# Kernel tuning notes

Hardware: AMD Instinct MI355X
Metric: run time of the kernel (lower is better)

Reference implementation:

```python
import jax, jax.numpy as jnp
import numpy as np

B, T, E = 8, 2048, 1024  # batch, seq_len, emb_size (= output_emb_size)


def setup_inputs() -> dict:
    key = jax.random.key(0)
    k1, k2, k3, k4, k5, k6, k7 = jax.random.split(key, 7)
    return {
        "q": jax.random.normal(k1, (B, T, E), jnp.float32),
        "k": jax.random.normal(k2, (B, T, E), jnp.float32),
        "v": jax.random.normal(k3, (B, T, E), jnp.float32),
        "mask": jax.random.randint(k4, (T, T), 0, 2, jnp.int32),
        # nn.Linear weights, stored [out, in] as in torch; applied as x @ W.T
        "Wq": jax.random.normal(k5, (E, E), jnp.float32) / np.sqrt(E),
        "Wk": jax.random.normal(k6, (E, E), jnp.float32) / np.sqrt(E),
        "Wv": jax.random.normal(k7, (E, E), jnp.float32) / np.sqrt(E),
    }


def reference(q, k, v, mask, Wq, Wk, Wv):
    # QKV projections (bias-free Linear): x @ W.T
    query = jnp.einsum("bte,oe->bto", q, Wq)
    key_p = jnp.einsum("bse,oe->bso", k, Wk)
    value = jnp.einsum("bse,oe->bso", v, Wv)
    d = key_p.shape[-1]
    scores = jnp.einsum("bto,bso->bts", query, key_p) / np.sqrt(d).astype(jnp.float32)
    # torch.any(mask): mask is nonzero somewhere -> apply masked_fill(mask==0, -inf)
    scores = jnp.where(mask[None, :, :] == 0, -jnp.inf, scores)
    weights = jax.nn.softmax(scores, axis=-1)
    return jnp.einsum("bts,bso->bto", weights, value)
```

## Files before the change

### kernel.cpp

```cpp
#include <hip/hip_runtime.h>
#include <hip/hip_bf16.h>

typedef __attribute__((ext_vector_type(8))) short short8;
typedef __attribute__((ext_vector_type(8))) unsigned short ushortx8;
typedef __attribute__((ext_vector_type(4))) unsigned short ushortx4;
typedef __attribute__((ext_vector_type(4))) float floatx4;

#define NB 8
#define NT 2048
#define NE 1024

__device__ __forceinline__ unsigned short f2bf(float f){
  unsigned int u = __builtin_bit_cast(unsigned int, f);
  u += 0x7FFFu + ((u >> 16) & 1u);
  return (unsigned short)(u >> 16);
}
__device__ __forceinline__ float bf2f(unsigned short h){
  unsigned int u = ((unsigned int)h) << 16;
  return __builtin_bit_cast(float, u);
}

__device__ __forceinline__ void async16(void* lds, const void* g){
  __builtin_amdgcn_global_load_lds(
      (const __attribute__((address_space(1))) unsigned int*)g,
      (__attribute__((address_space(3))) unsigned int*)lds, 16, 0, 0);
}

#define MFMA16(d, va, vb) \
  d = __builtin_amdgcn_mfma_f32_16x16x32_bf16(va, vb, d, 0, 0, 0)

__global__ __launch_bounds__(256) void cvt3(const float* __restrict__ a0,
                                            const float* __restrict__ a1,
                                            const float* __restrict__ a2,
                                            unsigned short* __restrict__ out,
                                            int n4_per){
  const float* src = blockIdx.y == 0 ? a0 : (blockIdx.y == 1 ? a1 : a2);
  unsigned short* dst = out + (size_t)blockIdx.y * (size_t)n4_per * 4;
  int i = blockIdx.x * 256 + threadIdx.x;
  if (i < n4_per){
    floatx4 f = ((const floatx4*)src)[i];
    ushortx4 o;
    o.x = f2bf(f.x); o.y = f2bf(f.y); o.z = f2bf(f.z); o.w = f2bf(f.w);
    *(ushortx4*)(dst + (size_t)i * 4) = o;
  }
}

__global__ __launch_bounds__(256) void pack_mask(const int* __restrict__ m,
                                                 unsigned long long* __restrict__ bits){
  int t = blockIdx.x * 256 + threadIdx.x;
  const int4* p = (const int4*)(m + (size_t)t * 64);
  unsigned long long w = 0;
  #pragma unroll
  for (int jj = 0; jj < 16; jj++){
    int4 v = p[jj];
    w |= (unsigned long long)(v.x != 0) << (jj * 4 + 0);
    w |= (unsigned long long)(v.y != 0) << (jj * 4 + 1);
    w |= (unsigned long long)(v.z != 0) << (jj * 4 + 2);
    w |= (unsigned long long)(v.w != 0) << (jj * 4 + 3);
  }
  bits[t] = w;
}

template<int EPI>
__global__ __launch_bounds__(512, 2) void gemm_nt(
    const unsigned short* __restrict__ A, long strideA,
    const unsigned short* __restrict__ B, long strideB,
    void* __restrict__ Out, long strideOutBytes,
    const unsigned long long* __restrict__ mbits,
    float* __restrict__ rowsums,
    int K, int gx, int gy)
{
  __shared__ __attribute__((aligned(16))) char Lds[131072];
  const int tid = threadIdx.x;
  const int lane = tid & 63, wave = tid >> 6;

  int L = blockIdx.x;
  int xcd = L & 7, tt = L >> 3;
  int x = tt % gx;
  int strip = xcd + ((tt / gx) << 3);
  int y = strip % gy, z = strip / gy;
  const int m0 = y << 8, n0 = x << 8;
  const int Nn = gx << 8;

  const unsigned short* Az = A + (size_t)z * strideA;
  const unsigned short* Bz = B + (size_t)z * strideB;

  const long rowb  = (long)K * 2;
  const long rs128 = rowb << 7;
  const int r0 = tid >> 2;
  const int c0 = (tid & 3) ^ ((r0 >> 1) & 3);
  const char* pA0 = (const char*)Az + (size_t)(m0 + r0) * rowb + (c0 << 4);
  const char* pA1 = pA0 + 64;
  const char* pB0 = (const char*)Bz + (size_t)(n0 + r0) * rowb + (c0 << 4);
  const char* pB1 = pB0 + 64;
  const int stg = tid << 4;

  auto stageU = [&](const char*& g, int ldsoff){
    async16(Lds + ldsoff + stg,        g);
    async16(Lds + ldsoff + stg + 8192, g + rs128);
    g += 128;
  };

  const int lm = lane & 15, qd = lane >> 4;
  const int wm = wave >> 2, wn = wave & 3;
  const int fsw  = (qd ^ ((lm >> 1) & 3)) << 4;
  const int aoff = ((wm << 7) + lm) * 64 + fsw;
  const int boff = 32768 + ((wn << 6) + lm) * 64 + fsw;

  floatx4 acc[8][4];
  floatx4 zero4 = {0.f, 0.f, 0.f, 0.f};
  #pragma unroll
  for (int a = 0; a < 8; a++)
    #pragma unroll
    for (int b = 0; b < 4; b++) acc[a][b] = zero4;

  const int NK = K >> 6;

  stageU(pB0, 32768);
  stageU(pA0, 0);
  stageU(pB1, 32768 + 16384);
  stageU(pA1, 16384);
  stageU(pB0, 65536 + 32768);
  stageU(pA0, 65536);
  stageU(pB1, 65536 + 32768 + 16384);
  asm volatile("s_waitcnt vmcnt(6)\n\ts_barrier" ::: "memory");

  short8 a[4], b[4];
  for (int t = 0; t < NK; ++t){
    const int rb = (t & 1) << 16;
    const int sb = rb ^ 65536;

    if (t + 1 < NK) stageU(pA1, sb + 16384);
    #pragma unroll
    for (int j = 0; j < 4; j++) a[j] = *(const short8*)(Lds + rb + aoff + j * 1024);
    #pragma unroll
    for (int n = 0; n < 4; n++) b[n] = *(const short8*)(Lds + rb + boff + n * 1024);
    asm volatile("s_waitcnt lgkmcnt(0)\n\ts_barrier" ::: "memory");
    __builtin_amdgcn_sched_barrier(0);
    __builtin_amdgcn_s_setprio(1);
    #pragma unroll
    for (int j = 0; j < 4; j++)
      #pragma unroll
      for (int n = 0; n < 4; n++) MFMA16(acc[j][n], a[j], b[n]);
    __builtin_amdgcn_s_setprio(0);

    if (t + 2 < NK) stageU(pB0, rb + 32768);
    #pragma unroll
    for (int j = 0; j < 4; j++) a[j] = *(const short8*)(Lds + rb + aoff + (4 + j) * 1024);
    if (t + 2 < NK)
      asm volatile("s_waitcnt vmcnt(10) lgkmcnt(0)\n\ts_barrier" ::: "memory");
    else if (t + 1 < NK)
      asm volatile("s_waitcnt vmcnt(8) lgkmcnt(0)\n\ts_barrier" ::: "memory");
    else
      asm volatile("s_waitcnt lgkmcnt(0)\n\ts_barrier" ::: "memory");
    __builtin_amdgcn_sched_barrier(0);
    __builtin_amdgcn_s_setprio(1);
    #pragma unroll
    for (int j = 0; j < 4; j++)
      #pragma unroll
      for (int n = 0; n < 4; n++) MFMA16(acc[4 + j][n], a[j], b[n]);
    __builtin_amdgcn_s_setprio(0);

    if (t + 2 < NK) stageU(pA0, rb);
    #pragma unroll
    for (int j = 0; j < 4; j++) a[j] = *(const short8*)(Lds + rb + 16384 + aoff + j * 1024);
    #pragma unroll
    for (int n = 0; n < 4; n++) b[n] = *(const short8*)(Lds + rb + 16384 + boff + n * 1024);
    asm volatile("s_waitcnt lgkmcnt(0)\n\ts_barrier" ::: "memory");
    __builtin_amdgcn_sched_barrier(0);
    __builtin_amdgcn_s_setprio(1);
    #pragma unroll
    for (int j = 0; j < 4; j++)
      #pragma unroll
      for (int n = 0; n < 4; n++) MFMA16(acc[j][n], a[j], b[n]);
    __builtin_amdgcn_s_setprio(0);

    #pragma unroll
    for (int j = 0; j < 4; j++) a[j] = *(const short8*)(Lds + rb + 16384 + aoff + (4 + j) * 1024);
    if (t + 2 < NK){
      stageU(pB1, rb + 32768 + 16384);
      asm volatile("s_waitcnt vmcnt(8) lgkmcnt(0)\n\ts_barrier" ::: "memory");
    } else {
      asm volatile("s_waitcnt vmcnt(0) lgkmcnt(0)\n\ts_barrier" ::: "memory");
    }
    __builtin_amdgcn_sched_barrier(0);
    __builtin_amdgcn_s_setprio(1);
    #pragma unroll
    for (int j = 0; j < 4; j++)
      #pragma unroll
      for (int n = 0; n < 4; n++) MFMA16(acc[4 + j][n], a[j], b[n]);
    __builtin_amdgcn_s_setprio(0);
  }

  char* OutZ = (char*)Out + (size_t)z * strideOutBytes;
  const int colbase = n0 + (wn << 6);
  if constexpr (EPI == 1){
    const int wcol = colbase >> 6;
    #pragma unroll
    for (int mi = 0; mi < 8; mi++){
      #pragma unroll
      for (int i = 0; i < 4; i++){
        int row = m0 + (wm << 7) + mi * 16 + qd * 4 + i;
        unsigned long long w = mbits[(size_t)row * (NT / 64) + wcol];
        unsigned short* po = (unsigned short*)OutZ + (size_t)row * Nn + colbase;
        float rsum = 0.f;
        #pragma unroll
        for (int ni = 0; ni < 4; ni++){
          float vv = acc[mi][ni][i];
          float e = ((w >> (ni * 16 + lm)) & 1ull) ? __expf(vv * 0.03125f) : 0.f;
          rsum += e;
          po[ni * 16 + lm] = f2bf(e);
        }
        rsum += __shfl_xor(rsum, 1, 64);
        rsum += __shfl_xor(rsum, 2, 64);
        rsum += __shfl_xor(rsum, 4, 64);
        rsum += __shfl_xor(rsum, 8, 64);
        if (lm == 0) atomicAdd(rowsums + ((size_t)z << 11) + row, rsum);
      }
    }
  } else if constexpr (EPI == 2){
    #pragma unroll
    for (int mi = 0; mi < 8; mi++){
      #pragma unroll
      for (int i = 0; i < 4; i++){
        int row = m0 + (wm << 7) + mi * 16 + qd * 4 + i;
        float inv = 1.0f / rowsums[((size_t)z << 11) + row];
        #pragma unroll
        for (int ni = 0; ni < 4; ni++){
          int col = colbase + ni * 16 + lm;
          ((float*)OutZ)[(size_t)row * Nn + col] = acc[mi][ni][i] * inv;
        }
      }
    }
  } else {
    #pragma unroll
    for (int mi = 0; mi < 8; mi++){
      #pragma unroll
      for (int i = 0; i < 4; i++){
        int row = m0 + (wm << 7) + mi * 16 + qd * 4 + i;
        #pragma unroll
        for (int ni = 0; ni < 4; ni++){
          int col = colbase + ni * 16 + lm;
          ((unsigned short*)OutZ)[(size_t)row * Nn + col] = f2bf(acc[mi][ni][i]);
        }
      }
    }
  }
}

__global__ __launch_bounds__(256) void transpose_bf16(const unsigned short* __restrict__ in,
                                                      unsigned short* __restrict__ out,
                                                      float* __restrict__ rowsums,
                                                      int rows, int cols){
  __shared__ __attribute__((aligned(16))) unsigned short tile[64][72];
  const unsigned short* ib = in + (size_t)blockIdx.z * rows * cols;
  unsigned short* ob = out + (size_t)blockIdx.z * rows * cols;
  int r0 = blockIdx.x * 64;
  int c0 = blockIdx.y * 64;
  int tid = threadIdx.x;
  if (blockIdx.x == 0 && blockIdx.y == 0){
    float* rz = rowsums + ((size_t)blockIdx.z << 11);
    #pragma unroll
    for (int i = 0; i < 8; i++) rz[tid + i * 256] = 0.f;
  }
  #pragma unroll
  for (int i = 0; i < 2; i++){
    int id = tid + i * 256;
    int r = id >> 3, c = (id & 7) * 8;
    ushortx8 v = *(const ushortx8*)(ib + (size_t)(r0 + r) * cols + c0 + c);
    *(ushortx8*)&tile[r][c] = v;
  }
  __syncthreads();
  #pragma unroll
  for (int i = 0; i < 2; i++){
    int id = tid + i * 256;
    int r = id >> 3, c = (id & 7) * 8;
    ushortx8 v;
    #pragma unroll
    for (int j = 0; j < 8; j++) v[j] = tile[c + j][r];
    *(ushortx8*)(ob + (size_t)(c0 + r) * rows + r0 + c) = v;
  }
}

extern "C" void kernel_launch(void* const* d_in, const int* in_sizes, int n_in,
                              void* d_out, int out_size, void* d_ws, size_t ws_size,
                              hipStream_t stream){
  const float* q  = (const float*)d_in[0];
  const float* k  = (const float*)d_in[1];
  const float* v  = (const float*)d_in[2];
  const int* mask = (const int*)d_in[3];
  const float* Wq = (const float*)d_in[4];
  const float* Wk = (const float*)d_in[5];
  const float* Wv = (const float*)d_in[6];

  const size_t BTE = (size_t)NB * NT * NE;
  unsigned short* ws   = (unsigned short*)d_ws;
  unsigned short* QKVp = ws;
  unsigned short* VpT  = ws + 3 * BTE;
  unsigned short* Sb   = ws + 3 * BTE + BTE;
  unsigned short* Qin  = ws + 3 * BTE;
  unsigned short* Wb   = ws + 3 * BTE + BTE + (size_t)NB * NT * NT;
  unsigned long long* mbits = (unsigned long long*)(Wb + (size_t)3 * NE * NE);
  float* rowsums = (float*)Wb;

  unsigned short* Qp = QKVp;
  unsigned short* Kp = QKVp + BTE;
  unsigned short* Vp = QKVp + 2 * BTE;

  cvt3<<<dim3(16384, 3), 256, 0, stream>>>(q, k, v, Qin, (int)(BTE / 4));
  cvt3<<<dim3(1024, 3), 256, 0, stream>>>(Wq, Wk, Wv, Wb, NE * NE / 4);
  pack_mask<<<256, 256, 0, stream>>>(mask, mbits);

  gemm_nt<0><<<768, 512, 0, stream>>>(
      Qin, (long)BTE, Wb, (long)NE * NE,
      QKVp, (long)BTE * 2, nullptr, nullptr, NE, 4, 64);

  transpose_bf16<<<dim3(32, 16, 8), 256, 0, stream>>>(Vp, VpT, rowsums, NT, NE);

  gemm_nt<1><<<512, 512, 0, stream>>>(
      Qp, (long)NT * NE, Kp, (long)NT * NE,
      Sb, (long)NT * NT * 2, mbits, rowsums, NE, 8, 8);

  gemm_nt<2><<<256, 512, 0, stream>>>(
      Sb, (long)NT * NT, VpT, (long)NE * NT,
      d_out, (long)NT * NE * 4, nullptr, rowsums, NT, 4, 8);
}
```

Before: 513.3 us.

## Fuse V transpose into projection GEMM epilogue and merge prep kernels

The projection GEMM now writes the V tile transposed through LDS directly into the V^T buffer, which removes the separate transpose kernel and its extra read and write of V. Weight conversion and mask packing are merged into one launch, and rowsum zeroing moves to a hipMemsetAsync. LDS grows to hold the padded transpose tile, which may affect occupancy, and the transposed store adds a barrier to the epilogue.

```diff
diff --git a/kernel.cpp b/kernel.cpp
--- a/kernel.cpp
+++ b/kernel.cpp
@@ -5,6 +5,7 @@
 typedef __attribute__((ext_vector_type(8))) unsigned short ushortx8;
 typedef __attribute__((ext_vector_type(4))) unsigned short ushortx4;
 typedef __attribute__((ext_vector_type(4))) float floatx4;
+typedef __attribute__((ext_vector_type(2))) unsigned int uint2v;
 
 #define NB 8
 #define NT 2048
@@ -14,10 +15,6 @@
   unsigned int u = __builtin_bit_cast(unsigned int, f);
   u += 0x7FFFu + ((u >> 16) & 1u);
   return (unsigned short)(u >> 16);
-}
-__device__ __forceinline__ float bf2f(unsigned short h){
-  unsigned int u = ((unsigned int)h) << 16;
-  return __builtin_bit_cast(float, u);
 }
 
 __device__ __forceinline__ void async16(void* lds, const void* g){
@@ -45,20 +42,35 @@
   }
 }
 
-__global__ __launch_bounds__(256) void pack_mask(const int* __restrict__ m,
-                                                 unsigned long long* __restrict__ bits){
-  int t = blockIdx.x * 256 + threadIdx.x;
-  const int4* p = (const int4*)(m + (size_t)t * 64);
-  unsigned long long w = 0;
-  #pragma unroll
-  for (int jj = 0; jj < 16; jj++){
-    int4 v = p[jj];
-    w |= (unsigned long long)(v.x != 0) << (jj * 4 + 0);
-    w |= (unsigned long long)(v.y != 0) << (jj * 4 + 1);
-    w |= (unsigned long long)(v.z != 0) << (jj * 4 + 2);
-    w |= (unsigned long long)(v.w != 0) << (jj * 4 + 3);
+__global__ __launch_bounds__(256) void prep(const float* __restrict__ w0,
+                                            const float* __restrict__ w1,
+                                            const float* __restrict__ w2,
+                                            unsigned short* __restrict__ wout,
+                                            const int* __restrict__ m,
+                                            unsigned long long* __restrict__ bits){
+  int bx = blockIdx.x;
+  if (bx < 3072){
+    int y = bx >> 10;
+    int i = ((bx & 1023) << 8) + threadIdx.x;
+    const float* src = y == 0 ? w0 : (y == 1 ? w1 : w2);
+    floatx4 f = ((const floatx4*)src)[i];
+    ushortx4 o;
+    o.x = f2bf(f.x); o.y = f2bf(f.y); o.z = f2bf(f.z); o.w = f2bf(f.w);
+    *(ushortx4*)(wout + (size_t)y * (NE * NE) + (size_t)i * 4) = o;
+  } else {
+    int t = ((bx - 3072) << 8) + threadIdx.x;
+    const int4* p = (const int4*)(m + (size_t)t * 64);
+    unsigned long long w = 0;
+    #pragma unroll
+    for (int jj = 0; jj < 16; jj++){
+      int4 v = p[jj];
+      w |= (unsigned long long)(v.x != 0) << (jj * 4 + 0);
+      w |= (unsigned long long)(v.y != 0) << (jj * 4 + 1);
+      w |= (unsigned long long)(v.z != 0) << (jj * 4 + 2);
+      w |= (unsigned long long)(v.w != 0) << (jj * 4 + 3);
+    }
+    bits[t] = w;
   }
-  bits[t] = w;
 }
 
 template<int EPI>
@@ -68,9 +80,10 @@
     void* __restrict__ Out, long strideOutBytes,
     const unsigned long long* __restrict__ mbits,
     float* __restrict__ rowsums,
+    unsigned short* __restrict__ trOut,
     int K, int gx, int gy)
 {
-  __shared__ __attribute__((aligned(16))) char Lds[131072];
+  __shared__ __attribute__((aligned(16))) char Lds[135168];
   const int tid = threadIdx.x;
   const int lane = tid & 63, wave = tid >> 6;
 
@@ -233,52 +246,45 @@
       }
     }
   } else {
-    #pragma unroll
-    for (int mi = 0; mi < 8; mi++){
-      #pragma unroll
-      for (int i = 0; i < 4; i++){
-        int row = m0 + (wm << 7) + mi * 16 + qd * 4 + i;
+    if (trOut != nullptr && z == 2){
+      #pragma unroll
+      for (int mi = 0; mi < 8; mi++){
+        int row0 = (wm << 7) + mi * 16 + qd * 4;
         #pragma unroll
         for (int ni = 0; ni < 4; ni++){
-          int col = colbase + ni * 16 + lm;
-          ((unsigned short*)OutZ)[(size_t)row * Nn + col] = f2bf(acc[mi][ni][i]);
+          int col = (wn << 6) + ni * 16 + lm;
+          unsigned int lo = (unsigned int)f2bf(acc[mi][ni][0]) |
+                            ((unsigned int)f2bf(acc[mi][ni][1]) << 16);
+          unsigned int hi = (unsigned int)f2bf(acc[mi][ni][2]) |
+                            ((unsigned int)f2bf(acc[mi][ni][3]) << 16);
+          uint2v p; p.x = lo; p.y = hi;
+          *(uint2v*)(Lds + col * 528 + row0 * 2) = p;
         }
       }
-    }
-  }
-}
-
-__global__ __launch_bounds__(256) void transpose_bf16(const unsigned short* __restrict__ in,
-                                                      unsigned short* __restrict__ out,
-                                                      float* __restrict__ rowsums,
-                                                      int rows, int cols){
-  __shared__ __attribute__((aligned(16))) unsigned short tile[64][72];
-  const unsigned short* ib = in + (size_t)blockIdx.z * rows * cols;
-  unsigned short* ob = out + (size_t)blockIdx.z * rows * cols;
-  int r0 = blockIdx.x * 64;
-  int c0 = blockIdx.y * 64;
-  int tid = threadIdx.x;
-  if (blockIdx.x == 0 && blockIdx.y == 0){
-    float* rz = rowsums + ((size_t)blockIdx.z << 11);
-    #pragma unroll
-    for (int i = 0; i < 8; i++) rz[tid + i * 256] = 0.f;
-  }
-  #pragma unroll
-  for (int i = 0; i < 2; i++){
-    int id = tid + i * 256;
-    int r = id >> 3, c = (id & 7) * 8;
-    ushortx8 v = *(const ushortx8*)(ib + (size_t)(r0 + r) * cols + c0 + c);
-    *(ushortx8*)&tile[r][c] = v;
-  }
-  __syncthreads();
-  #pragma unroll
-  for (int i = 0; i < 2; i++){
-    int id = tid + i * 256;
-    int r = id >> 3, c = (id & 7) * 8;
-    ushortx8 v;
-    #pragma unroll
-    for (int j = 0; j < 8; j++) v[j] = tile[c + j][r];
-    *(ushortx8*)(ob + (size_t)(c0 + r) * rows + r0 + c) = v;
+      __syncthreads();
+      int bb = m0 >> 11, tb = m0 & 2047;
+      unsigned short* base = trOut + (size_t)bb * NE * NT + (size_t)n0 * NT + tb;
+      #pragma unroll
+      for (int k2 = 0; k2 < 16; k2++){
+        int gid = (k2 << 9) + tid;
+        int col = gid >> 5, chk = gid & 31;
+        ushortx8 vv = *(const ushortx8*)(Lds + col * 528 + (chk << 4));
+        *(ushortx8*)(base + (size_t)col * NT + (chk << 3)) = vv;
+      }
+    } else {
+      #pragma unroll
+      for (int mi = 0; mi < 8; mi++){
+        #pragma unroll
+        for (int i = 0; i < 4; i++){
+          int row = m0 + (wm << 7) + mi * 16 + qd * 4 + i;
+          #pragma unroll
+          for (int ni = 0; ni < 4; ni++){
+            int col = colbase + ni * 16 + lm;
+            ((unsigned short*)OutZ)[(size_t)row * Nn + col] = f2bf(acc[mi][ni][i]);
+          }
+        }
+      }
+    }
   }
 }
 
@@ -296,32 +302,30 @@
   const size_t BTE = (size_t)NB * NT * NE;
   unsigned short* ws   = (unsigned short*)d_ws;
   unsigned short* QKVp = ws;
-  unsigned short* VpT  = ws + 3 * BTE;
   unsigned short* Sb   = ws + 3 * BTE + BTE;
   unsigned short* Qin  = ws + 3 * BTE;
   unsigned short* Wb   = ws + 3 * BTE + BTE + (size_t)NB * NT * NT;
   unsigned long long* mbits = (unsigned long long*)(Wb + (size_t)3 * NE * NE);
   float* rowsums = (float*)Wb;
 
-  unsigned short* Qp = QKVp;
-  unsigned short* Kp = QKVp + BTE;
-  unsigned short* Vp = QKVp + 2 * BTE;
+  unsigned short* Qp  = QKVp;
+  unsigned short* Kp  = QKVp + BTE;
+  unsigned short* VpT = QKVp + 2 * BTE;
 
   cvt3<<<dim3(16384, 3), 256, 0, stream>>>(q, k, v, Qin, (int)(BTE / 4));
-  cvt3<<<dim3(1024, 3), 256, 0, stream>>>(Wq, Wk, Wv, Wb, NE * NE / 4);
-  pack_mask<<<256, 256, 0, stream>>>(mask, mbits);
+  prep<<<3328, 256, 0, stream>>>(Wq, Wk, Wv, Wb, mask, mbits);
 
   gemm_nt<0><<<768, 512, 0, stream>>>(
       Qin, (long)BTE, Wb, (long)NE * NE,
-      QKVp, (long)BTE * 2, nullptr, nullptr, NE, 4, 64);
-
-  transpose_bf16<<<dim3(32, 16, 8), 256, 0, stream>>>(Vp, VpT, rowsums, NT, NE);
+      QKVp, (long)BTE * 2, nullptr, nullptr, VpT, NE, 4, 64);
+
+  hipMemsetAsync(rowsums, 0, (size_t)NB * NT * sizeof(float), stream);
 
   gemm_nt<1><<<512, 512, 0, stream>>>(
       Qp, (long)NT * NE, Kp, (long)NT * NE,
-      Sb, (long)NT * NT * 2, mbits, rowsums, NE, 8, 8);
+      Sb, (long)NT * NT * 2, mbits, rowsums, nullptr, NE, 8, 8);
 
   gemm_nt<2><<<256, 512, 0, stream>>>(
       Sb, (long)NT * NT, VpT, (long)NE * NT,
-      d_out, (long)NT * NE * 4, nullptr, rowsums, NT, 4, 8);
-}
+      d_out, (long)NT * NE * 4, nullptr, rowsums, nullptr, NT, 4, 8);
+}
```

Result: faster. 498.1 us (-3.0%).
